# Optimization experiments

Measured on AMD Instinct MI355X. Metric: run time of the kernel, lower is better.

The kernel has to match this reference:

```python
import jax, jax.numpy as jnp
import numpy as np

N_NODES = 100_000
N_EDGES = 1_600_000
N_SPECIES = 4
ATTR = 16
HID = 32
NBASIS = 8
SH = 4  # l=0 (1) + l=1 (3)
R_CUT = 5.0


def setup_inputs() -> dict:
    key = jax.random.key(0)
    ks = jax.random.split(key, 13)
    inp = {
        "x": jax.random.randint(ks[0], (N_NODES,), 0, N_SPECIES),
        "pos": jax.random.normal(ks[1], (N_NODES, 3), jnp.float32),
        "edge_index": jax.random.randint(ks[2], (2, N_EDGES), 0, N_NODES),
        "cell": jax.random.normal(ks[3], (3, 3), jnp.float32),
        "cell_offset": jax.random.randint(ks[4], (N_EDGES, 3), 0, 3),
        "elem_embed": jax.random.normal(ks[5], (N_SPECIES, ATTR), jnp.float32),
        "W_embed": jax.random.normal(ks[6], (ATTR, HID), jnp.float32) * 0.25,
        "Wr": jax.random.normal(ks[7], (3, NBASIS, HID * SH), jnp.float32) * 0.25,
        "br": jax.random.normal(ks[8], (3, HID * SH), jnp.float32) * 0.1,
        "Wout": jax.random.normal(ks[9], (3, HID, HID), jnp.float32) * 0.18,
        "Wsc": jax.random.normal(ks[10], (3, ATTR, HID), jnp.float32) * 0.25,
        "P1": jax.random.normal(ks[11], (HID, 32), jnp.float32) * 0.18,
        "P2": jax.random.normal(ks[12], (32, 4), jnp.float32) * 0.18,
    }
    return inp


def _radial_basis(r, r_safe):
    # Bessel basis with smooth polynomial cutoff (p = 6)
    n = jnp.arange(1, NBASIS + 1, dtype=r.dtype)  # [NBASIS]
    rb = jnp.sin(n * jnp.pi * r / R_CUT) / r_safe  # [E, NBASIS]
    u = r / R_CUT
    p = 6.0
    env = 1.0 - (p + 1) * (p + 2) / 2 * u ** p + p * (p + 2) * u ** (p + 1) - p * (p + 1) / 2 * u ** (p + 2)
    env = jnp.where(u < 1.0, env, 0.0)
    return rb * env


def reference(x, pos, edge_index, cell, cell_offset, elem_embed, W_embed, Wr, br, Wout, Wsc, P1, P2):
    src, dst = edge_index[0], edge_index[1]
    n_nodes = pos.shape[0]
    n_edges = src.shape[0]

    # PBC shift vectors (offsets in {-1,0,1})
    period_vec = (cell_offset.astype(pos.dtype) - 1.0) @ cell  # [E,3]

    # node attributes / initial embedding
    x_attr = elem_embed[x]          # [N, ATTR]
    h = x_attr @ W_embed            # [N, HID]

    # edge attributes: vectors, lengths, spherical harmonics (l<=1)
    edge_vec = pos[dst] - pos[src] + period_vec            # [E,3]
    r = jnp.linalg.norm(edge_vec, axis=-1, keepdims=True)  # [E,1]
    r_safe = jnp.maximum(r, 1e-9)
    unit = edge_vec / r_safe
    edge_sh = jnp.concatenate([jnp.ones_like(r), unit], axis=-1)  # [E,SH]

    rbf = _radial_basis(r, r_safe)  # [E, NBASIS]

    # 3 message-passing convolutions
    for l in range(3):
        w = (rbf @ Wr[l] + br[l]).reshape(n_edges, HID, SH)          # per-edge TP weights
        msg = jnp.einsum('eh,es,ehs->eh', h[src], edge_sh, w)        # gather + edge compute
        agg = jax.ops.segment_sum(msg, dst, num_segments=n_nodes)    # scatter-reduce
        h = jax.nn.silu(agg @ Wout[l] + x_attr @ Wsc[l])

    # post-conv readout
    h = jax.nn.silu(h @ P1) @ P2  # [N,4]
    energies = h[:, 0]
    forces = h[:, 1:4]
    return energies, forces
```

## Files before the change

### kernel.cpp

```cpp
#include <hip/hip_runtime.h>
#include <hip/hip_bf16.h>
#include <math.h>

#define NN 100000
#define NE 1600000
#define HIDD 32
#define ATTR_ 16
#define NB 8
#define NBUK 782
#define CAP 2560
#define WPB 10
#define SCHUNK 4096
#define PAD_PAY (13<<17)

typedef __hip_bfloat16 bf16;
typedef _Float16 half8  __attribute__((ext_vector_type(8)));
typedef _Float16 half4v __attribute__((ext_vector_type(4)));
typedef _Float16 half2v __attribute__((ext_vector_type(2)));
typedef float    f32x4  __attribute__((ext_vector_type(4)));

__device__ __forceinline__ float silu_(float v){ return v / (1.f + expf(-v)); }

__global__ void k_init(const int* __restrict__ x, const float* __restrict__ elem,
                       const float* __restrict__ Wemb, bf16* __restrict__ h,
                       float* __restrict__ agg){
  int idx = blockIdx.x*256 + threadIdx.x;
  if (idx >= NN*HIDD) return;
  int node = idx >> 5, hh = idx & 31;
  int xi = x[node];
  float acc = 0.f;
  #pragma unroll
  for (int a=0; a<ATTR_; a++) acc += elem[xi*ATTR_+a] * Wemb[a*HIDD+hh];
  h[idx] = __float2bfloat16(acc);
  agg[idx] = 0.f;
}

__global__ void k_binit(int* __restrict__ bcur){
  int i = blockIdx.x*256 + threadIdx.x;
  if (i < NBUK) bcur[i] = i*CAP;
}

__global__ void __launch_bounds__(256) k_bscatter(
    const int* __restrict__ ei, const int* __restrict__ coff,
    int* __restrict__ bcur, int* __restrict__ pairs){
  __shared__ int lh[NBUK];
  __shared__ int gb[NBUK];
  __shared__ int sbr[SCHUNK];
  __shared__ int spay[SCHUNK];
  const int t = threadIdx.x;
  const int base = blockIdx.x * SCHUNK;
  for (int i=t; i<NBUK; i+=256) lh[i] = 0;
  __syncthreads();
  for (int rr=0; rr<SCHUNK; rr+=256){
    int e = base + rr + t;
    if (e < NE){
      int src = ei[e], dst = ei[NE + e];
      int code = coff[e*3+0] + 3*coff[e*3+1] + 9*coff[e*3+2];
      int b = dst >> 7;
      int rank = atomicAdd(&lh[b], 1);
      sbr[rr+t]  = (b<<16) | rank;
      spay[rr+t] = src | (code<<17) | ((dst & 127)<<22);
    }
  }
  __syncthreads();
  for (int i=t; i<NBUK; i+=256){
    int c = lh[i];
    gb[i] = c ? atomicAdd(&bcur[i], c) : 0;
  }
  __syncthreads();
  for (int rr=0; rr<SCHUNK; rr+=256){
    int e = base + rr + t;
    if (e < NE){
      int br = sbr[rr+t];
      int b = br >> 16;
      int p = gb[b] + (br & 0xFFFF);
      if (p < (b+1)*CAP) pairs[p] = spay[rr+t];
    }
  }
}

__global__ void __launch_bounds__(256) k_fsort(
    const int* __restrict__ pairs, const int* __restrict__ bcur,
    int* __restrict__ es){
  __shared__ int spay[CAP];
  __shared__ int hist[128];
  __shared__ int cur[128];
  const int b = blockIdx.x, t = threadIdx.x;
  const int base = b*CAP;
  int K = bcur[b] - base; if (K > CAP) K = CAP; if (K < 0) K = 0;
  if (t < 128) hist[t] = 0;
  __syncthreads();
  for (int i=t; i<K; i+=256){
    int pay = pairs[base + i];
    spay[i] = pay;
    atomicAdd(&hist[(pay>>22) & 127], 1);
  }
  __syncthreads();
  if (t < 128) cur[t] = hist[t];
  __syncthreads();
  #pragma unroll
  for (int off=1; off<128; off<<=1){
    int u = (t >= off && t < 128) ? cur[t-off] : 0;
    __syncthreads();
    if (t < 128) cur[t] += u;
    __syncthreads();
  }
  if (t < 128) cur[t] -= hist[t];
  __syncthreads();
  for (int i=t; i<K; i+=256){
    int pay = spay[i];
    int p = base + atomicAdd(&cur[(pay>>22) & 127], 1);
    es[p] = pay;
  }
  for (int i=K+t; i<CAP; i+=256) es[base+i] = PAD_PAY;
}

__global__ void __launch_bounds__(256) k_edge6(
    const int* __restrict__ es, const int* __restrict__ bcur,
    const float* __restrict__ pos, const float* __restrict__ cell,
    const float* __restrict__ Wr_l, const float* __restrict__ br_l,
    const bf16* __restrict__ h, float* __restrict__ agg){
  __shared__ _Float16 Gs[256][40];
  __shared__ float ssh[256][4];
  __shared__ int ssrc[256];
  __shared__ int sdst[256];
  __shared__ _Float16 W2T[32][32];
  __shared__ float scell[9];
  _Float16 (*Gs2)[260] = reinterpret_cast<_Float16 (*)[260]>(&Gs[0][0]);

  const int t = threadIdx.x;
  int blk;
  {
    const int nwg = gridDim.x;
    int q = nwg >> 3, r = nwg & 7;
    int xcd = blockIdx.x & 7, lidx = blockIdx.x >> 3;
    blk = (xcd < r) ? (xcd*(q+1) + lidx) : (r*(q+1) + (xcd-r)*q + lidx);
  }
  const int b = blk / WPB, w = blk - b*WPB;
  const int base0 = b*CAP;
  int K = bcur[b] - base0; if (K > CAP) K = CAP;
  const int rem = K - w*256;
  if (rem <= 0) return;
  const int remc = rem < 256 ? rem : 256;

  if (t < 9) scell[t] = cell[t];
  {
    int hh2 = t >> 3, kq = t & 7;
    float4 w4 = *reinterpret_cast<const float4*>(Wr_l + kq*128 + hh2*4);
    W2T[hh2][kq*4+0] = (_Float16)w4.x;
    W2T[hh2][kq*4+1] = (_Float16)w4.y;
    W2T[hh2][kq*4+2] = (_Float16)w4.z;
    W2T[hh2][kq*4+3] = (_Float16)w4.w;
  }

  const int j = base0 + w*256 + t;
  const int pay = es[j];
  const int srcn = pay & 0x1FFFF;
  const int dstn = (b<<7) + ((pay>>22) & 127);
  ssrc[t] = srcn; sdst[t] = dstn;
  float pdx = pos[dstn*3+0], pdy = pos[dstn*3+1], pdz = pos[dstn*3+2];
  float psx = pos[srcn*3+0], psy = pos[srcn*3+1], psz = pos[srcn*3+2];
  const int wv = t >> 6, l = t & 63, lrow = l & 15, lk = l >> 4;
  float4 br0 = *reinterpret_cast<const float4*>(br_l + 4*lrow);
  float4 br1 = *reinterpret_cast<const float4*>(br_l + 4*(16+lrow));
  __syncthreads();

  const int g = t >> 5, hh = t & 31, base = g*32;
  const unsigned short* hu = reinterpret_cast<const unsigned short*>(h);
  unsigned short hb[32];
  #pragma unroll
  for (int k=0; k<32; k++)
    hb[k] = hu[(size_t)ssrc[base+k]*HIDD + hh];

  {
    int code = (pay >> 17) & 31;
    int q = code / 3;
    float c0 = (float)(code - 3*q - 1);
    float c1 = (float)(q - 3*(q/3) - 1);
    float c2 = (float)(q/3 - 1);
    float vx = pdx - psx + c0*scell[0]+c1*scell[3]+c2*scell[6];
    float vy = pdy - psy + c0*scell[1]+c1*scell[4]+c2*scell[7];
    float vz = pdz - psz + c0*scell[2]+c1*scell[5]+c2*scell[8];
    float r  = sqrtf(vx*vx + vy*vy + vz*vz);
    float rs = fmaxf(r, 1e-9f);
    float u  = r * 0.2f;
    float env = 0.f;
    if (u < 1.f){
      float u2=u*u, u3=u2*u, u6=u3*u3, u7=u6*u, u8=u7*u;
      env = 1.f - 28.f*u6 + 48.f*u7 - 21.f*u8;
    }
    float sc = env / rs;
    float s1, c1t;
    __sincosf(0.62831853071795864769f * r, &s1, &c1t);
    float twoc = 2.f*c1t;
    float inv = 1.f / rs;
    float ux = vx*inv, uy = vy*inv, uz = vz*inv;
    float sp = 0.f, sn = s1;
    #pragma unroll
    for (int bb=0; bb<NB; bb++){
      float rb = sn*sc;
      half2v p0 = { (_Float16)rb,      (_Float16)(rb*ux) };
      half2v p1 = { (_Float16)(rb*uy), (_Float16)(rb*uz) };
      *reinterpret_cast<half2v*>(&Gs[t][bb*4])   = p0;
      *reinterpret_cast<half2v*>(&Gs[t][bb*4+2]) = p1;
      float nx = twoc*sn - sp; sp = sn; sn = nx;
    }
    float4 sh4 = make_float4(1.f, ux, uy, uz);
    *reinterpret_cast<float4*>(ssh[t]) = sh4;
  }

  asm volatile("s_waitcnt lgkmcnt(0)" ::: "memory");
  __builtin_amdgcn_s_barrier();
  __builtin_amdgcn_sched_barrier(0);

  half8 a[4];
  #pragma unroll
  for (int m=0; m<4; m++)
    a[m] = *reinterpret_cast<half8*>(&Gs[(wv*4+m)*16 + lrow][lk*8]);
  half8 b0h = *reinterpret_cast<half8*>(&W2T[lrow][lk*8]);
  half8 b1h = *reinterpret_cast<half8*>(&W2T[16+lrow][lk*8]);
  asm volatile("s_waitcnt lgkmcnt(0)" ::: "memory");
  __builtin_amdgcn_s_barrier();
  __builtin_amdgcn_sched_barrier(0);
  {
    const f32x4 zz = {0.f,0.f,0.f,0.f};
    #pragma unroll
    for (int m=0; m<4; m++){
      f32x4 c0 = __builtin_amdgcn_mfma_f32_16x16x32_f16(a[m], b0h, zz, 0, 0, 0);
      f32x4 c1 = __builtin_amdgcn_mfma_f32_16x16x32_f16(a[m], b1h, zz, 0, 0, 0);
      #pragma unroll
      for (int r=0; r<4; r++){
        int edge = wv*64 + m*16 + lk*4 + r;
        float4 sh4 = *reinterpret_cast<float4*>(ssh[edge]);
        float bias0 = sh4.x*br0.x + sh4.y*br0.y + sh4.z*br0.z + sh4.w*br0.w;
        float bias1 = sh4.x*br1.x + sh4.y*br1.y + sh4.z*br1.z + sh4.w*br1.w;
        Gs2[lrow][edge]    = (_Float16)(c0[r] + bias0);
        Gs2[16+lrow][edge] = (_Float16)(c1[r] + bias1);
      }
    }
  }

  half4v cv[8];
  #pragma unroll
  for (int q=0; q<8; q++)
    cv[q] = *reinterpret_cast<half4v*>(&Gs2[hh][base + q*4]);
  float accv = 0.f;
  int curd = sdst[base];
  #pragma unroll
  for (int k=0; k<32; k++){
    const int idx = base + k;
    int dst = sdst[idx];
    bool ok = idx < remc;
    if (ok && dst != curd){ atomicAdd(agg + (size_t)curd*HIDD + hh, accv); accv = 0.f; curd = dst; }
    float hv = __uint_as_float(((unsigned)hb[k]) << 16);
    float cvf = (float)cv[k>>2][k&3];
    if (ok) accv += hv * cvf;
  }
  if (accv != 0.f) atomicAdd(agg + (size_t)curd*HIDD + hh, accv);
}

__global__ void __launch_bounds__(256) k_edge(
    const float* __restrict__ pos, const int* __restrict__ ei,
    const float* __restrict__ cell, const int* __restrict__ coff,
    const float* __restrict__ Wr_l, const float* __restrict__ br_l,
    const bf16* __restrict__ h, float* __restrict__ agg){
  __shared__ float sfeat[8][12];
  __shared__ int   snode[8][2];
  const int e0 = blockIdx.x * 8;
  const int t  = threadIdx.x;
  if (t < 8){
    int e = e0 + t;
    int src = ei[e], dst = ei[NE + e];
    snode[t][0] = src; snode[t][1] = dst;
    float c0 = (float)(coff[e*3+0] - 1);
    float c1 = (float)(coff[e*3+1] - 1);
    float c2 = (float)(coff[e*3+2] - 1);
    float vx = pos[dst*3+0]-pos[src*3+0] + c0*cell[0]+c1*cell[3]+c2*cell[6];
    float vy = pos[dst*3+1]-pos[src*3+1] + c0*cell[1]+c1*cell[4]+c2*cell[7];
    float vz = pos[dst*3+2]-pos[src*3+2] + c0*cell[2]+c1*cell[5]+c2*cell[8];
    float r  = sqrtf(vx*vx+vy*vy+vz*vz);
    float rs = fmaxf(r, 1e-9f);
    float u  = r * 0.2f;
    float env = 0.f;
    if (u < 1.f){
      float u2=u*u, u3=u2*u, u6=u3*u3, u7=u6*u, u8=u7*u;
      env = 1.f - 28.f*u6 + 48.f*u7 - 21.f*u8;
    }
    float sc = env / rs;
    #pragma unroll
    for (int b=0; b<NB; b++)
      sfeat[t][b] = sinf((float)(b+1) * 3.14159265358979323846f * u) * sc;
    float inv = 1.f / rs;
    sfeat[t][8]  = 1.f;
    sfeat[t][9]  = vx*inv;
    sfeat[t][10] = vy*inv;
    sfeat[t][11] = vz*inv;
  }
  __syncthreads();
  const int el = t >> 5, hh = t & 31;
  const int src = snode[el][0], dst = snode[el][1];
  float hs = __bfloat162float(h[(size_t)src*HIDD + hh]);
  float4 acc = *reinterpret_cast<const float4*>(br_l + 4*hh);
  #pragma unroll
  for (int b=0; b<NB; b++){
    float rb = sfeat[el][b];
    float4 w = *reinterpret_cast<const float4*>(Wr_l + b*128 + 4*hh);
    acc.x += rb*w.x; acc.y += rb*w.y; acc.z += rb*w.z; acc.w += rb*w.w;
  }
  float c = acc.x*sfeat[el][8] + acc.y*sfeat[el][9]
          + acc.z*sfeat[el][10] + acc.w*sfeat[el][11];
  atomicAdd(agg + (size_t)dst*HIDD + hh, hs*c);
}

__global__ void k_node(const int* __restrict__ x, const float* __restrict__ elem,
                       const float* __restrict__ Wout_l, const float* __restrict__ Wsc_l,
                       bf16* __restrict__ h, float* __restrict__ agg){
  int idx = blockIdx.x*256 + threadIdx.x;
  if (idx >= NN*HIDD) return;
  int node = idx >> 5, hh = idx & 31;
  int xi = x[node];
  const float* arow = agg + (size_t)node*HIDD;
  float acc = 0.f;
  #pragma unroll
  for (int i=0; i<HIDD; i++) acc += arow[i] * Wout_l[i*HIDD+hh];
  #pragma unroll
  for (int a=0; a<ATTR_; a++) acc += elem[xi*ATTR_+a] * Wsc_l[a*HIDD+hh];
  h[idx] = __float2bfloat16(silu_(acc));
  agg[idx] = 0.f;
}

__global__ void __launch_bounds__(256) k_final2(
    const bf16* __restrict__ h, const float* __restrict__ P1,
    const float* __restrict__ P2, float* __restrict__ out){
  __shared__ float sP1[32][32];
  __shared__ float sh[8][32];
  const int t = threadIdx.x;
  {
    float4 v = reinterpret_cast<const float4*>(P1)[t];
    int r = (t*4) >> 5, c = (t*4) & 31;
    sP1[r][c]   = v.x; sP1[r][c+1] = v.y;
    sP1[r][c+2] = v.z; sP1[r][c+3] = v.w;
  }
  const int node0 = blockIdx.x * 8;
  ((float*)sh)[t] = __bfloat162float(h[(size_t)node0*HIDD + t]);
  __syncthreads();
  const int g = t >> 5, j = t & 31;
  const int node = node0 + g;
  float tj = 0.f;
  #pragma unroll
  for (int i=0; i<32; i++) tj += sh[g][i] * sP1[i][j];
  tj = silu_(tj);
  float4 p2 = reinterpret_cast<const float4*>(P2)[j];
  float o0 = tj*p2.x, o1 = tj*p2.y, o2 = tj*p2.z, o3 = tj*p2.w;
  #pragma unroll
  for (int m=1; m<32; m<<=1){
    o0 += __shfl_xor(o0, m);
    o1 += __shfl_xor(o1, m);
    o2 += __shfl_xor(o2, m);
    o3 += __shfl_xor(o3, m);
  }
  if (j == 0){
    out[node]            = o0;
    out[NN + node*3 + 0] = o1;
    out[NN + node*3 + 1] = o2;
    out[NN + node*3 + 2] = o3;
  }
}

extern "C" void kernel_launch(void* const* d_in, const int* in_sizes, int n_in,
                              void* d_out, int out_size, void* d_ws, size_t ws_size,
                              hipStream_t stream){
  const int*   x    = (const int*)  d_in[0];
  const float* pos  = (const float*)d_in[1];
  const int*   ei   = (const int*)  d_in[2];
  const float* cell = (const float*)d_in[3];
  const int*   coff = (const int*)  d_in[4];
  const float* elem = (const float*)d_in[5];
  const float* Wemb = (const float*)d_in[6];
  const float* Wr   = (const float*)d_in[7];
  const float* br   = (const float*)d_in[8];
  const float* Wout = (const float*)d_in[9];
  const float* Wsc  = (const float*)d_in[10];
  const float* P1   = (const float*)d_in[11];
  const float* P2   = (const float*)d_in[12];
  float* out = (float*)d_out;

  char* w = (char*)d_ws;
  bf16*  h    = (bf16*)w;  w += (size_t)NN*HIDD*2;
  float* agg  = (float*)w; w += (size_t)NN*HIDD*4;
  int*   bcur = (int*)w;   w += (size_t)1024*4;
  int*   es   = (int*)w;   w += (size_t)NBUK*CAP*4;
  const size_t need = (size_t)(w - (char*)d_ws);
  const bool fast = (ws_size >= need);
  int* pairs = (int*)agg;

  if (fast){
    k_binit<<<(NBUK+255)/256, 256, 0, stream>>>(bcur);
    k_bscatter<<<(NE + SCHUNK-1)/SCHUNK, 256, 0, stream>>>(ei, coff, bcur, pairs);
    k_fsort<<<NBUK, 256, 0, stream>>>(pairs, bcur, es);
  }
  k_init<<<(NN*HIDD+255)/256, 256, 0, stream>>>(x, elem, Wemb, h, agg);
  for (int l=0; l<3; l++){
    if (fast){
      k_edge6<<<NBUK*WPB, 256, 0, stream>>>(es, bcur, pos, cell,
                                            Wr + (size_t)l*NB*HIDD*4, br + (size_t)l*HIDD*4,
                                            h, agg);
    } else {
      k_edge<<<NE/8, 256, 0, stream>>>(pos, ei, cell, coff,
                                       Wr + (size_t)l*NB*HIDD*4, br + (size_t)l*HIDD*4,
                                       h, agg);
    }
    k_node<<<(NN*HIDD+255)/256, 256, 0, stream>>>(x, elem,
                                       Wout + (size_t)l*HIDD*HIDD, Wsc + (size_t)l*ATTR_*HIDD,
                                       h, agg);
  }
  k_final2<<<NN/8, 256, 0, stream>>>(h, P1, P2, out);
}
```

Baseline: 335.5 us.

## Make edge kernel wave-local: drop block barriers and shared weight staging

The edge kernel now loads the radial weight fragments straight from global memory into MFMA operand registers and reads the cell matrix directly, so it no longer stages them in shared memory. Because each wave only touches its own 64 edge rows in shared memory, all block-wide barriers are removed. The per-edge weights are written back in place into the same row-major buffer instead of a transposed one. Gains should come from removing synchronization and shared-memory staging. The cost is more redundant global weight loads per thread, plus a reliance on implicit intra-wave ordering for correctness.

```diff
diff --git a/kernel.cpp b/kernel.cpp
--- a/kernel.cpp
+++ b/kernel.cpp
@@ -15,7 +15,6 @@
 
 typedef __hip_bfloat16 bf16;
 typedef _Float16 half8  __attribute__((ext_vector_type(8)));
-typedef _Float16 half4v __attribute__((ext_vector_type(4)));
 typedef _Float16 half2v __attribute__((ext_vector_type(2)));
 typedef float    f32x4  __attribute__((ext_vector_type(4)));
 
@@ -115,7 +114,7 @@
   for (int i=K+t; i<CAP; i+=256) es[base+i] = PAD_PAY;
 }
 
-__global__ void __launch_bounds__(256) k_edge6(
+__global__ void __launch_bounds__(256) k_edge7(
     const int* __restrict__ es, const int* __restrict__ bcur,
     const float* __restrict__ pos, const float* __restrict__ cell,
     const float* __restrict__ Wr_l, const float* __restrict__ br_l,
@@ -124,9 +123,6 @@
   __shared__ float ssh[256][4];
   __shared__ int ssrc[256];
   __shared__ int sdst[256];
-  __shared__ _Float16 W2T[32][32];
-  __shared__ float scell[9];
-  _Float16 (*Gs2)[260] = reinterpret_cast<_Float16 (*)[260]>(&Gs[0][0]);
 
   const int t = threadIdx.x;
   int blk;
@@ -143,15 +139,7 @@
   if (rem <= 0) return;
   const int remc = rem < 256 ? rem : 256;
 
-  if (t < 9) scell[t] = cell[t];
-  {
-    int hh2 = t >> 3, kq = t & 7;
-    float4 w4 = *reinterpret_cast<const float4*>(Wr_l + kq*128 + hh2*4);
-    W2T[hh2][kq*4+0] = (_Float16)w4.x;
-    W2T[hh2][kq*4+1] = (_Float16)w4.y;
-    W2T[hh2][kq*4+2] = (_Float16)w4.z;
-    W2T[hh2][kq*4+3] = (_Float16)w4.w;
-  }
+  const int wv = t >> 6, l = t & 63, lrow = l & 15, lk = l >> 4;
 
   const int j = base0 + w*256 + t;
   const int pay = es[j];
@@ -160,10 +148,16 @@
   ssrc[t] = srcn; sdst[t] = dstn;
   float pdx = pos[dstn*3+0], pdy = pos[dstn*3+1], pdz = pos[dstn*3+2];
   float psx = pos[srcn*3+0], psy = pos[srcn*3+1], psz = pos[srcn*3+2];
-  const int wv = t >> 6, l = t & 63, lrow = l & 15, lk = l >> 4;
+  float4 wA0 = *reinterpret_cast<const float4*>(Wr_l + (2*lk+0)*128 + lrow*4);
+  float4 wA1 = *reinterpret_cast<const float4*>(Wr_l + (2*lk+1)*128 + lrow*4);
+  float4 wB0 = *reinterpret_cast<const float4*>(Wr_l + (2*lk+0)*128 + (16+lrow)*4);
+  float4 wB1 = *reinterpret_cast<const float4*>(Wr_l + (2*lk+1)*128 + (16+lrow)*4);
+  half8 b0h = { (_Float16)wA0.x,(_Float16)wA0.y,(_Float16)wA0.z,(_Float16)wA0.w,
+                (_Float16)wA1.x,(_Float16)wA1.y,(_Float16)wA1.z,(_Float16)wA1.w };
+  half8 b1h = { (_Float16)wB0.x,(_Float16)wB0.y,(_Float16)wB0.z,(_Float16)wB0.w,
+                (_Float16)wB1.x,(_Float16)wB1.y,(_Float16)wB1.z,(_Float16)wB1.w };
   float4 br0 = *reinterpret_cast<const float4*>(br_l + 4*lrow);
   float4 br1 = *reinterpret_cast<const float4*>(br_l + 4*(16+lrow));
-  __syncthreads();
 
   const int g = t >> 5, hh = t & 31, base = g*32;
   const unsigned short* hu = reinterpret_cast<const unsigned short*>(h);
@@ -178,9 +172,9 @@
     float c0 = (float)(code - 3*q - 1);
     float c1 = (float)(q - 3*(q/3) - 1);
     float c2 = (float)(q/3 - 1);
-    float vx = pdx - psx + c0*scell[0]+c1*scell[3]+c2*scell[6];
-    float vy = pdy - psy + c0*scell[1]+c1*scell[4]+c2*scell[7];
-    float vz = pdz - psz + c0*scell[2]+c1*scell[5]+c2*scell[8];
+    float vx = pdx - psx + c0*cell[0]+c1*cell[3]+c2*cell[6];
+    float vy = pdy - psy + c0*cell[1]+c1*cell[4]+c2*cell[7];
+    float vz = pdz - psz + c0*cell[2]+c1*cell[5]+c2*cell[8];
     float r  = sqrtf(vx*vx + vy*vy + vz*vz);
     float rs = fmaxf(r, 1e-9f);
     float u  = r * 0.2f;
@@ -209,41 +203,25 @@
     *reinterpret_cast<float4*>(ssh[t]) = sh4;
   }
 
-  asm volatile("s_waitcnt lgkmcnt(0)" ::: "memory");
-  __builtin_amdgcn_s_barrier();
-  __builtin_amdgcn_sched_barrier(0);
-
-  half8 a[4];
-  #pragma unroll
-  for (int m=0; m<4; m++)
-    a[m] = *reinterpret_cast<half8*>(&Gs[(wv*4+m)*16 + lrow][lk*8]);
-  half8 b0h = *reinterpret_cast<half8*>(&W2T[lrow][lk*8]);
-  half8 b1h = *reinterpret_cast<half8*>(&W2T[16+lrow][lk*8]);
-  asm volatile("s_waitcnt lgkmcnt(0)" ::: "memory");
-  __builtin_amdgcn_s_barrier();
-  __builtin_amdgcn_sched_barrier(0);
   {
     const f32x4 zz = {0.f,0.f,0.f,0.f};
     #pragma unroll
     for (int m=0; m<4; m++){
-      f32x4 c0 = __builtin_amdgcn_mfma_f32_16x16x32_f16(a[m], b0h, zz, 0, 0, 0);
-      f32x4 c1 = __builtin_amdgcn_mfma_f32_16x16x32_f16(a[m], b1h, zz, 0, 0, 0);
+      half8 a = *reinterpret_cast<half8*>(&Gs[wv*64 + m*16 + lrow][lk*8]);
+      f32x4 c0 = __builtin_amdgcn_mfma_f32_16x16x32_f16(a, b0h, zz, 0, 0, 0);
+      f32x4 c1 = __builtin_amdgcn_mfma_f32_16x16x32_f16(a, b1h, zz, 0, 0, 0);
       #pragma unroll
       for (int r=0; r<4; r++){
         int edge = wv*64 + m*16 + lk*4 + r;
         float4 sh4 = *reinterpret_cast<float4*>(ssh[edge]);
         float bias0 = sh4.x*br0.x + sh4.y*br0.y + sh4.z*br0.z + sh4.w*br0.w;
         float bias1 = sh4.x*br1.x + sh4.y*br1.y + sh4.z*br1.z + sh4.w*br1.w;
-        Gs2[lrow][edge]    = (_Float16)(c0[r] + bias0);
-        Gs2[16+lrow][edge] = (_Float16)(c1[r] + bias1);
+        Gs[edge][lrow]    = (_Float16)(c0[r] + bias0);
+        Gs[edge][16+lrow] = (_Float16)(c1[r] + bias1);
       }
     }
   }
 
-  half4v cv[8];
-  #pragma unroll
-  for (int q=0; q<8; q++)
-    cv[q] = *reinterpret_cast<half4v*>(&Gs2[hh][base + q*4]);
   float accv = 0.f;
   int curd = sdst[base];
   #pragma unroll
@@ -253,7 +231,7 @@
     bool ok = idx < remc;
     if (ok && dst != curd){ atomicAdd(agg + (size_t)curd*HIDD + hh, accv); accv = 0.f; curd = dst; }
     float hv = __uint_as_float(((unsigned)hb[k]) << 16);
-    float cvf = (float)cv[k>>2][k&3];
+    float cvf = (float)Gs[idx][hh];
     if (ok) accv += hv * cvf;
   }
   if (accv != 0.f) atomicAdd(agg + (size_t)curd*HIDD + hh, accv);
@@ -402,7 +380,7 @@
   k_init<<<(NN*HIDD+255)/256, 256, 0, stream>>>(x, elem, Wemb, h, agg);
   for (int l=0; l<3; l++){
     if (fast){
-      k_edge6<<<NBUK*WPB, 256, 0, stream>>>(es, bcur, pos, cell,
+      k_edge7<<<NBUK*WPB, 256, 0, stream>>>(es, bcur, pos, cell,
                                             Wr + (size_t)l*NB*HIDD*4, br + (size_t)l*HIDD*4,
                                             h, agg);
     } else {
```

Result: slower. 355.8 us (+6.0%).
